# Kernel optimization log

Hardware: AMD Instinct MI355X
Metric: run time of the kernel (lower is better)

Reference implementation:

```python
import jax, jax.numpy as jnp
import numpy as np

MARGIN = 0.3
NUM_CLASSES = 1000


def setup_inputs() -> dict:
    key = jax.random.key(0)
    k1, k2 = jax.random.split(key)
    B, D = 8192, 256
    inputs = jax.random.normal(k1, (B, D), dtype=jnp.float32)
    targets = jax.random.randint(k2, (B,), 0, NUM_CLASSES, dtype=jnp.int64)
    return {"inputs": inputs, "targets": targets}


def reference(inputs, targets):
    # Squared Euclidean pairwise distances: ||x_i||^2 + ||x_j||^2 - 2 x_i.x_j
    sq = jnp.sum(inputs * inputs, axis=1)                      # [B]
    dist = sq[:, None] + sq[None, :] - 2.0 * (inputs @ inputs.T)  # [B, B]

    # Hard mining: per-row max over positives (same label, incl. self),
    # min over negatives, exactly as the torch per-row masked max/min loop.
    pos_mask = targets[:, None] == targets[None, :]            # [B, B] bool
    neg_inf = jnp.float32(-jnp.inf)
    pos_inf = jnp.float32(jnp.inf)
    dist_ap = jnp.max(jnp.where(pos_mask, dist, neg_inf), axis=1)  # [B]
    dist_an = jnp.min(jnp.where(pos_mask, pos_inf, dist), axis=1)  # [B]

    # MarginRankingLoss(margin)(dist_an, dist_ap, y=1) = mean relu(ap - an + m)
    loss = jnp.mean(jax.nn.relu(dist_ap - dist_an + MARGIN))
    prec = jnp.mean((dist_an > dist_ap).astype(jnp.float32))
    return (loss, prec)
```

## Files before the change

### kernel.cpp

```cpp
#include <hip/hip_runtime.h>
#include <hip/hip_bf16.h>

#define B_N 8192
#define D_K 256
#define MARGIN 0.3f
#define NBLK 2080

typedef float f32x4 __attribute__((ext_vector_type(4)));
typedef short s16x8 __attribute__((ext_vector_type(8)));

__device__ __forceinline__ unsigned fkey(float f) {
    unsigned u = __float_as_uint(f);
    return (u & 0x80000000u) ? ~u : (u | 0x80000000u);
}
__device__ __forceinline__ float kval(unsigned k) {
    return (k & 0x80000000u) ? __uint_as_float(k ^ 0x80000000u)
                             : __uint_as_float(~k);
}

__device__ __forceinline__ void load_lds16(const unsigned short* g,
                                           unsigned short* l) {
    __builtin_amdgcn_global_load_lds(
        (const __attribute__((address_space(1))) unsigned int*)g,
        (__attribute__((address_space(3))) unsigned int*)l, 16, 0, 0);
}

__global__ __launch_bounds__(256) void prep_kernel(const float* __restrict__ X,
        float* __restrict__ sq, unsigned* __restrict__ apk,
        unsigned* __restrict__ ank, unsigned short* __restrict__ Xp,
        float* __restrict__ acc2) {
    int row  = (blockIdx.x << 2) + (threadIdx.x >> 6);
    int lane = threadIdx.x & 63;
    const float4 v = reinterpret_cast<const float4*>(X + (size_t)row * D_K)[lane];

    float xs[4] = {v.x, v.y, v.z, v.w};
    ushort4 hv;
    unsigned short* hp = &hv.x;
    float s = 0.f;
    #pragma unroll
    for (int i = 0; i < 4; ++i) {
        __hip_bfloat16 h = __float2bfloat16(xs[i]);
        hp[i] = *reinterpret_cast<unsigned short*>(&h);
        float hf = __bfloat162float(h);
        s = fmaf(hf, hf, s);
    }
    *reinterpret_cast<ushort4*>(Xp + (size_t)row * D_K + lane * 4) = hv;

    #pragma unroll
    for (int o = 32; o > 0; o >>= 1) s += __shfl_down(s, o, 64);
    if (lane == 0) {
        sq[row]  = s;
        apk[row] = 0u;
        ank[row] = 0xFFFFFFFFu;
    }
    if (blockIdx.x == 0 && threadIdx.x == 0) {
        acc2[0] = 0.f; acc2[1] = 0.f;
        reinterpret_cast<unsigned*>(acc2)[2] = 0u;
    }
}

#define BM 128
#define BN 128

__global__ __launch_bounds__(256, 4) void dist_kernel(
        const unsigned short* __restrict__ Xp,
        const int* __restrict__ tgt, const float* __restrict__ sq,
        unsigned* __restrict__ apk, unsigned* __restrict__ ank) {
    __shared__ unsigned short Ab[2][128 * 32];
    __shared__ unsigned short Bb[2][128 * 32];

    const int t    = threadIdx.x;
    const int lane = t & 63;
    const int wave = t >> 6;
    const int wrow = (wave >> 1) * 64;
    const int wcol = (wave & 1) * 64;
    const int fr   = lane & 15;
    const int quad = lane >> 4;
    const float INF = __int_as_float(0x7f800000);

    int tt = blockIdx.x;
    int bx = (int)((sqrtf(8.f * (float)tt + 1.f) - 1.f) * 0.5f);
    while ((bx + 1) * (bx + 2) / 2 <= tt) ++bx;
    while (bx * (bx + 1) / 2 > tt) --bx;
    int by = tt - bx * (bx + 1) / 2;
    const int bm = by * BM;
    const int bn = bx * BN;

    const unsigned short* ag[2];
    const unsigned short* bg[2];
    int ldso[2];
    #pragma unroll
    for (int j = 0; j < 2; ++j) {
        int g = wave * 64 + j * 256 + lane;
        int r = g >> 2, u = g & 3;
        ag[j] = Xp + (size_t)(bm + r) * D_K + u * 8;
        bg[j] = Xp + (size_t)(bn + r) * D_K + u * 8;
        ldso[j] = g * 8;
    }

    f32x4 acc[4][4];
    #pragma unroll
    for (int i = 0; i < 4; ++i)
        #pragma unroll
        for (int j = 0; j < 4; ++j) acc[i][j] = (f32x4){0.f, 0.f, 0.f, 0.f};

    #pragma unroll
    for (int j = 0; j < 2; ++j) {
        load_lds16(ag[j], &Ab[0][ldso[j]]);
        load_lds16(bg[j], &Bb[0][ldso[j]]);
    }

    #pragma unroll 1
    for (int w = 0; w < 8; ++w) {
        __syncthreads();
        if (w < 7) {
            const int ko = (w + 1) * 32;
            #pragma unroll
            for (int j = 0; j < 2; ++j) {
                load_lds16(ag[j] + ko, &Ab[(w + 1) & 1][ldso[j]]);
                load_lds16(bg[j] + ko, &Bb[(w + 1) & 1][ldso[j]]);
            }
        }
        const unsigned short* At = Ab[w & 1];
        const unsigned short* Bt = Bb[w & 1];

        s16x8 a[4], b[4];
        #pragma unroll
        for (int mi = 0; mi < 4; ++mi)
            a[mi] = *reinterpret_cast<const s16x8*>(
                &At[(wrow + mi * 16 + fr) * 32 + quad * 8]);
        #pragma unroll
        for (int ni = 0; ni < 4; ++ni)
            b[ni] = *reinterpret_cast<const s16x8*>(
                &Bt[(wcol + ni * 16 + fr) * 32 + quad * 8]);
        #pragma unroll
        for (int mi = 0; mi < 4; ++mi)
            #pragma unroll
            for (int ni = 0; ni < 4; ++ni)
                acc[mi][ni] = __builtin_amdgcn_mfma_f32_16x16x32_bf16(
                    a[mi], b[ni], acc[mi][ni], 0, 0, 0);
    }

    int   ct[4]; float csq[4];
    #pragma unroll
    for (int ni = 0; ni < 4; ++ni) {
        int c = bn + wcol + ni * 16 + fr;
        ct[ni] = tgt[c]; csq[ni] = sq[c];
    }
    float cap[4], can[4];
    #pragma unroll
    for (int ni = 0; ni < 4; ++ni) { cap[ni] = -INF; can[ni] = INF; }

    #pragma unroll
    for (int mi = 0; mi < 4; ++mi) {
        #pragma unroll
        for (int reg = 0; reg < 4; ++reg) {
            int rl = wrow + mi * 16 + quad * 4 + reg;
            int rt = tgt[bm + rl]; float rsq = sq[bm + rl];
            float rap = -INF, ran = INF;
            #pragma unroll
            for (int ni = 0; ni < 4; ++ni) {
                float d = rsq + csq[ni] - 2.f * acc[mi][ni][reg];
                bool pos = (rt == ct[ni]);
                if (pos) { rap = fmaxf(rap, d); cap[ni] = fmaxf(cap[ni], d); }
                else     { ran = fminf(ran, d); can[ni] = fminf(can[ni], d); }
            }
            #pragma unroll
            for (int o = 1; o < 16; o <<= 1) {
                rap = fmaxf(rap, __shfl_xor(rap, o, 64));
                ran = fminf(ran, __shfl_xor(ran, o, 64));
            }
            if (fr == 0) {
                atomicMax(&apk[bm + rl], fkey(rap));
                atomicMin(&ank[bm + rl], fkey(ran));
            }
        }
    }
    #pragma unroll
    for (int ni = 0; ni < 4; ++ni) {
        #pragma unroll
        for (int o = 16; o < 64; o <<= 1) {
            cap[ni] = fmaxf(cap[ni], __shfl_xor(cap[ni], o, 64));
            can[ni] = fminf(can[ni], __shfl_xor(can[ni], o, 64));
        }
    }
    if (lane < 16) {
        #pragma unroll
        for (int ni = 0; ni < 4; ++ni) {
            int c = bn + wcol + ni * 16 + lane;
            atomicMax(&apk[c], fkey(cap[ni]));
            atomicMin(&ank[c], fkey(can[ni]));
        }
    }
}

__global__ __launch_bounds__(256) void final_kernel(const unsigned* __restrict__ apk,
        const unsigned* __restrict__ ank, float* __restrict__ acc2,
        float* __restrict__ out) {
    __shared__ float s_sum[4], s_cnt[4];
    int i = blockIdx.x * 256 + threadIdx.x;
    float ap = kval(apk[i]);
    float an = kval(ank[i]);
    float v  = ap - an + MARGIN;
    float sum = v > 0.f ? v : 0.f;
    float cnt = an > ap ? 1.f : 0.f;
    #pragma unroll
    for (int o = 32; o > 0; o >>= 1) {
        sum += __shfl_down(sum, o, 64);
        cnt += __shfl_down(cnt, o, 64);
    }
    int wave = threadIdx.x >> 6, lane = threadIdx.x & 63;
    if (lane == 0) { s_sum[wave] = sum; s_cnt[wave] = cnt; }
    __syncthreads();
    if (threadIdx.x == 0) {
        float ts = 0.f, tc = 0.f;
        #pragma unroll
        for (int w = 0; w < 4; ++w) { ts += s_sum[w]; tc += s_cnt[w]; }
        atomicAdd(&acc2[0], ts);
        atomicAdd(&acc2[1], tc);
        __threadfence();
        unsigned ticket = atomicAdd(reinterpret_cast<unsigned*>(acc2) + 2, 1u);
        if (ticket == gridDim.x - 1) {
            float fs = atomicAdd(&acc2[0], 0.f);
            float fc = atomicAdd(&acc2[1], 0.f);
            out[0] = fs / (float)B_N;
            out[1] = fc / (float)B_N;
        }
    }
}

extern "C" void kernel_launch(void* const* d_in, const int* in_sizes, int n_in,
                              void* d_out, int out_size, void* d_ws, size_t ws_size,
                              hipStream_t stream) {
    const float* X   = (const float*)d_in[0];
    const int*   tgt = (const int*)d_in[1];

    char* ws = (char*)d_ws;
    float*          sq   = (float*)ws;
    unsigned*       apk  = (unsigned*)(ws + 32768);
    unsigned*       ank  = (unsigned*)(ws + 65536);
    float*          acc2 = (float*)(ws + 98304);
    unsigned short* Xp   = (unsigned short*)(ws + 131072);

    float* out = (float*)d_out;

    prep_kernel<<<B_N / 4, 256, 0, stream>>>(X, sq, apk, ank, Xp, acc2);
    dist_kernel<<<NBLK, 256, 0, stream>>>(Xp, tgt, sq, apk, ank);
    final_kernel<<<B_N / 256, 256, 0, stream>>>(apk, ank, acc2, out);
}
```

Baseline: 122.3 us.

## Swizzle LDS tile layout and use DPP row reductions in epilogue

```diff
diff --git a/kernel.cpp b/kernel.cpp
--- a/kernel.cpp
+++ b/kernel.cpp
@@ -23,6 +23,29 @@
     __builtin_amdgcn_global_load_lds(
         (const __attribute__((address_space(1))) unsigned int*)g,
         (__attribute__((address_space(3))) unsigned int*)l, 16, 0, 0);
+}
+
+__device__ __forceinline__ float rowred_max(float v) {
+    v = fmaxf(v, __int_as_float(__builtin_amdgcn_update_dpp(
+            __float_as_int(v), __float_as_int(v), 0x118, 0xF, 0xF, false)));
+    v = fmaxf(v, __int_as_float(__builtin_amdgcn_update_dpp(
+            __float_as_int(v), __float_as_int(v), 0x114, 0xF, 0xF, false)));
+    v = fmaxf(v, __int_as_float(__builtin_amdgcn_update_dpp(
+            __float_as_int(v), __float_as_int(v), 0x112, 0xF, 0xF, false)));
+    v = fmaxf(v, __int_as_float(__builtin_amdgcn_update_dpp(
+            __float_as_int(v), __float_as_int(v), 0x111, 0xF, 0xF, false)));
+    return v;
+}
+__device__ __forceinline__ float rowred_min(float v) {
+    v = fminf(v, __int_as_float(__builtin_amdgcn_update_dpp(
+            __float_as_int(v), __float_as_int(v), 0x118, 0xF, 0xF, false)));
+    v = fminf(v, __int_as_float(__builtin_amdgcn_update_dpp(
+            __float_as_int(v), __float_as_int(v), 0x114, 0xF, 0xF, false)));
+    v = fminf(v, __int_as_float(__builtin_amdgcn_update_dpp(
+            __float_as_int(v), __float_as_int(v), 0x112, 0xF, 0xF, false)));
+    v = fminf(v, __int_as_float(__builtin_amdgcn_update_dpp(
+            __float_as_int(v), __float_as_int(v), 0x111, 0xF, 0xF, false)));
+    return v;
 }
 
 __global__ __launch_bounds__(256) void prep_kernel(const float* __restrict__ X,
@@ -91,11 +114,12 @@
     int ldso[2];
     #pragma unroll
     for (int j = 0; j < 2; ++j) {
-        int g = wave * 64 + j * 256 + lane;
-        int r = g >> 2, u = g & 3;
-        ag[j] = Xp + (size_t)(bm + r) * D_K + u * 8;
-        bg[j] = Xp + (size_t)(bn + r) * D_K + u * 8;
-        ldso[j] = g * 8;
+        int S   = wave * 64 + j * 256 + lane;
+        int l   = S >> 3, idx = S & 7;
+        int u   = idx >> 1, r = l * 2 + (idx & 1);
+        ag[j]   = Xp + (size_t)(bm + r) * D_K + u * 8;
+        bg[j]   = Xp + (size_t)(bn + r) * D_K + u * 8;
+        ldso[j] = S * 8;
     }
 
     f32x4 acc[4][4];
@@ -126,13 +150,17 @@
 
         s16x8 a[4], b[4];
         #pragma unroll
-        for (int mi = 0; mi < 4; ++mi)
-            a[mi] = *reinterpret_cast<const s16x8*>(
-                &At[(wrow + mi * 16 + fr) * 32 + quad * 8]);
-        #pragma unroll
-        for (int ni = 0; ni < 4; ++ni)
-            b[ni] = *reinterpret_cast<const s16x8*>(
-                &Bt[(wcol + ni * 16 + fr) * 32 + quad * 8]);
+        for (int mi = 0; mi < 4; ++mi) {
+            int R = wrow + mi * 16 + fr;
+            int S = (R >> 1) * 8 + quad * 2 + (R & 1);
+            a[mi] = *reinterpret_cast<const s16x8*>(&At[S * 8]);
+        }
+        #pragma unroll
+        for (int ni = 0; ni < 4; ++ni) {
+            int R = wcol + ni * 16 + fr;
+            int S = (R >> 1) * 8 + quad * 2 + (R & 1);
+            b[ni] = *reinterpret_cast<const s16x8*>(&Bt[S * 8]);
+        }
         #pragma unroll
         for (int mi = 0; mi < 4; ++mi)
             #pragma unroll
@@ -165,12 +193,9 @@
                 if (pos) { rap = fmaxf(rap, d); cap[ni] = fmaxf(cap[ni], d); }
                 else     { ran = fminf(ran, d); can[ni] = fminf(can[ni], d); }
             }
-            #pragma unroll
-            for (int o = 1; o < 16; o <<= 1) {
-                rap = fmaxf(rap, __shfl_xor(rap, o, 64));
-                ran = fminf(ran, __shfl_xor(ran, o, 64));
-            }
-            if (fr == 0) {
+            rap = rowred_max(rap);
+            ran = rowred_min(ran);
+            if (fr == 15) {
                 atomicMax(&apk[bm + rl], fkey(rap));
                 atomicMin(&ank[bm + rl], fkey(ran));
             }
```

After: 120.2 us. No clear change (-1.7%).
